# Kernel tuning notes

Hardware: AMD Instinct MI355X
Metric: run time of the kernel (lower is better)

Reference implementation:

```python
import jax, jax.numpy as jnp
import numpy as np

VOCAB = 50257
HIDDEN = 4096
DH = 512
NUM_LAYERS = 2
NUM_DRAFT = 4


def setup_inputs() -> dict:
    key = jax.random.key(0)
    ks = jax.random.split(key, 16)
    B = 64
    s_ip = 1.0 / np.sqrt(HIDDEN)
    s_h = 1.0 / np.sqrt(DH)
    inp = {
        "hidden_state": jax.random.normal(ks[0], (B, HIDDEN), dtype=jnp.float32),
        "target_ids": jax.random.randint(ks[1], (B, NUM_DRAFT), 0, VOCAB),
        "ip_w": jax.random.normal(ks[2], (DH, HIDDEN), dtype=jnp.float32) * s_ip,
        "ip_b": jnp.zeros((DH,), dtype=jnp.float32),
        "w_ih0": jax.random.normal(ks[3], (3 * DH, DH), dtype=jnp.float32) * s_h,
        "w_hh0": jax.random.normal(ks[4], (3 * DH, DH), dtype=jnp.float32) * s_h,
        "b_ih0": jax.random.normal(ks[5], (3 * DH,), dtype=jnp.float32) * s_h,
        "b_hh0": jax.random.normal(ks[6], (3 * DH,), dtype=jnp.float32) * s_h,
        "w_ih1": jax.random.normal(ks[7], (3 * DH, DH), dtype=jnp.float32) * s_h,
        "w_hh1": jax.random.normal(ks[8], (3 * DH, DH), dtype=jnp.float32) * s_h,
        "b_ih1": jax.random.normal(ks[9], (3 * DH,), dtype=jnp.float32) * s_h,
        "b_hh1": jax.random.normal(ks[10], (3 * DH,), dtype=jnp.float32) * s_h,
        "embed": jax.random.normal(ks[11], (VOCAB, DH), dtype=jnp.float32),
        "out_w": jax.random.normal(ks[12], (VOCAB, DH), dtype=jnp.float32) * s_h,
    }
    return inp


def _gru_cell(x, h, w_ih, w_hh, b_ih, b_hh):
    # PyTorch GRU cell, gate order (r, z, n)
    gi = x @ w_ih.T + b_ih
    gh = h @ w_hh.T + b_hh
    ir, iz, inn = jnp.split(gi, 3, axis=-1)
    hr, hz, hn = jnp.split(gh, 3, axis=-1)
    r = jax.nn.sigmoid(ir + hr)
    z = jax.nn.sigmoid(iz + hz)
    n = jnp.tanh(inn + r * hn)
    return (1.0 - z) * n + z * h


def reference(hidden_state, target_ids, ip_w, ip_b, w_ih0, w_hh0, b_ih0, b_hh0,
              w_ih1, w_hh1, b_ih1, b_hh1, embed, out_w):
    B = hidden_state.shape[0]
    h0 = hidden_state @ ip_w.T + ip_b           # [B, DH]
    h = [h0, h0]                                # replicated over num_layers
    x = jnp.zeros((B, DH), dtype=hidden_state.dtype)
    logits_list = []
    for step in range(NUM_DRAFT):
        h1 = _gru_cell(x, h[0], w_ih0, w_hh0, b_ih0, b_hh0)
        h2 = _gru_cell(h1, h[1], w_ih1, w_hh1, b_ih1, b_hh1)
        h = [h1, h2]
        logits = h2 @ out_w.T                   # [B, VOCAB]
        logits_list.append(logits)
        x = embed[target_ids[:, step]]          # teacher-forced next input
    return jnp.stack(logits_list, axis=1)       # [B, NUM_DRAFT, VOCAB]
```

## Files before the change

### kernel.cpp

```cpp
#include <hip/hip_runtime.h>
#include <hip/hip_bf16.h>

#define B64   64
#define DH    512
#define HID   4096
#define VOC   50257
#define NSTEP 4
#define HSZ   (B64*DH)
#define NL0   64
#define NL1   64

typedef __attribute__((ext_vector_type(8)))  short bf16x8;
typedef __attribute__((ext_vector_type(4)))  float f32x4;
typedef __attribute__((ext_vector_type(16))) float f32x16;
typedef __hip_bfloat16 bf16;

__device__ __forceinline__ bf16x8 ldg8(const bf16* p) {
    return *reinterpret_cast<const bf16x8*>(p);
}
__device__ __forceinline__ short f2bf(float x) {
    bf16 h = __float2bfloat16(x);
    return *reinterpret_cast<short*>(&h);
}
__device__ __forceinline__ bf16x8 cvt8(const float* p) {
    f32x4 a = *reinterpret_cast<const f32x4*>(p);
    f32x4 b = *reinterpret_cast<const f32x4*>(p + 4);
    bf16x8 r;
    r[0] = f2bf(a[0]); r[1] = f2bf(a[1]); r[2] = f2bf(a[2]); r[3] = f2bf(a[3]);
    r[4] = f2bf(b[0]); r[5] = f2bf(b[1]); r[6] = f2bf(b[2]); r[7] = f2bf(b[3]);
    return r;
}
__device__ __forceinline__ float sigmf(float x) { return 1.f / (1.f + __expf(-x)); }
__device__ __forceinline__ f32x4 mfma16(bf16x8 a, bf16x8 b, f32x4 c) {
    return __builtin_amdgcn_mfma_f32_16x16x32_bf16(a, b, c, 0, 0, 0);
}

__global__ __launch_bounds__(512) void k_prep(
    const float* __restrict__ hs, const float* __restrict__ ipw,
    const float* __restrict__ wi0, const float* __restrict__ wh0,
    const float* __restrict__ wi1, const float* __restrict__ wh1,
    const float* __restrict__ embed, const int* __restrict__ tids,
    bf16* __restrict__ hsb, bf16* __restrict__ ipwb,
    bf16* __restrict__ w0i, bf16* __restrict__ w0h,
    bf16* __restrict__ w1i, bf16* __restrict__ w1h,
    bf16* __restrict__ xemb)
{
    int c = blockIdx.x * 512 + threadIdx.x;
    const float* src; bf16* dst;
    if      (c < 262144) { size_t t = c;           src = ipw + t*8; dst = ipwb + t*8; }
    else if (c < 294912) { size_t t = c - 262144;  src = hs  + t*8; dst = hsb  + t*8; }
    else if (c < 393216) { size_t t = c - 294912;  src = wi0 + t*8; dst = w0i + t*8; }
    else if (c < 491520) { size_t t = c - 393216;  src = wh0 + t*8; dst = w0h + t*8; }
    else if (c < 589824) { size_t t = c - 491520;  src = wi1 + t*8; dst = w1i + t*8; }
    else if (c < 688128) { size_t t = c - 589824;  src = wh1 + t*8; dst = w1h + t*8; }
    else {
        int t = c - 688128;
        int r = t >> 6, j = t & 63;
        int s = r >> 6, b = r & 63;
        int rid = tids[b * NSTEP + s];
        src = embed + (size_t)rid * DH + j * 8;
        dst = xemb  + (size_t)r   * DH + j * 8;
    }
    *reinterpret_cast<bf16x8*>(dst) = cvt8(src);
}

__device__ __forceinline__ void barwait(int* bar, int idx, int target) {
    if (threadIdx.x == 0) {
        while (__hip_atomic_load(&bar[idx], __ATOMIC_RELAXED, __HIP_MEMORY_SCOPE_AGENT) < target)
            __builtin_amdgcn_s_sleep(1);
        (void)__hip_atomic_load(&bar[idx], __ATOMIC_ACQUIRE, __HIP_MEMORY_SCOPE_AGENT);
    }
    __syncthreads();
}
__device__ __forceinline__ void barbump(int* bar, int idx) {
    __syncthreads();
    if (threadIdx.x == 0)
        __hip_atomic_fetch_add(&bar[idx], 1, __ATOMIC_RELEASE, __HIP_MEMORY_SCOPE_AGENT);
}

__global__ __launch_bounds__(512) void k_rec(
    const bf16* __restrict__ hsb, const bf16* __restrict__ ipwb, const float* __restrict__ ipb,
    const bf16* __restrict__ w0i, const bf16* __restrict__ w0h,
    const float* __restrict__ bi0, const float* __restrict__ bh0,
    const bf16* __restrict__ w1i, const bf16* __restrict__ w1h,
    const float* __restrict__ bi1, const float* __restrict__ bh1,
    const bf16* __restrict__ xemb,
    bf16* __restrict__ h0b3, bf16* __restrict__ h1b, bf16* __restrict__ hbig,
    int* __restrict__ bar)
{
    __shared__ __align__(16) char smem[131072];
    int tid = threadIdx.x, w = tid >> 6, lane = tid & 63;
    int lr = lane & 15, q = lane >> 4;
    int bid = blockIdx.x;
    bool isL0 = bid < NL0;
    int sub = isL0 ? bid : bid - NL0;
    int dt = sub >> 1, mh = sub & 1;
    int d0 = dt * 16, M0 = mh * 32;
    int mt = w >> 2, kc = w & 3;
    int m0 = M0 + mt * 16, ml = mt * 16;
    int d = d0 + lr;
    int row = m0 + q * 4 + kc;

    if (isL0) {
        float bR0 = bi0[d] + bh0[d], bZ0 = bi0[DH+d] + bh0[DH+d];
        float biN0 = bi0[2*DH+d],    bhN0 = bh0[2*DH+d];
        float* sG = (float*)(smem + 81920);
        f32x4 zero4 = {0.f,0.f,0.f,0.f};
        float h0st;

        {
            const bf16* arow = hsb  + (size_t)(m0 + lr) * HID + kc * 1024 + q * 8;
            const bf16* brow = ipwb + (size_t)(d0 + lr) * HID + kc * 1024 + q * 8;
            f32x4 acc = zero4;
#pragma unroll 8
            for (int k0 = 0; k0 < 1024; k0 += 32)
                acc = mfma16(ldg8(arow + k0), ldg8(brow + k0), acc);
#pragma unroll
            for (int r = 0; r < 4; ++r) sG[(w*4 + r)*64 + lane] = acc[r];
            __syncthreads();
            float S = 0.f;
#pragma unroll
            for (int j = 0; j < 4; ++j) S += sG[((mt*4 + j)*4 + kc)*64 + lane];
            float v = S + ipb[d];
            h0st = v;
            bf16 vb = __float2bfloat16(v);
            h0b3[row * DH + d] = vb;
            h1b[row * DH + d] = vb;
            __syncthreads();
        }

#pragma unroll
        for (int i = 0; i < 6; ++i) {
            int c = tid + 512*i;
            int g = c >> 10, r = (c >> 6) & 15, kg = c & 63;
            const bf16* src = w0h + ((size_t)(g*DH + d0 + r))*DH + kg*8;
            int dst = g*16384 + r*1024 + ((kg*16) ^ ((r & 7) << 4));
            *reinterpret_cast<bf16x8*>(smem + dst) = ldg8(src);
        }

        float giR[NSTEP] = {0,0,0,0}, giZ[NSTEP] = {0,0,0,0}, giN[NSTEP] = {0,0,0,0};
#pragma unroll
        for (int s = 1; s < NSTEP; ++s) {
            const bf16* xr = xemb + (size_t)((s-1)*B64 + m0 + lr)*DH + kc*128 + q*8;
#pragma unroll
            for (int g = 0; g < 3; ++g) {
                const bf16* wr = w0i + (size_t)(g*DH + d0 + lr)*DH + kc*128 + q*8;
                f32x4 a = zero4;
#pragma unroll
                for (int kt = 0; kt < 4; ++kt)
                    a = mfma16(ldg8(xr + kt*32), ldg8(wr + kt*32), a);
#pragma unroll
                for (int r = 0; r < 4; ++r) sG[((g*8 + w)*4 + r)*64 + lane] = a[r];
            }
            __syncthreads();
            float sR = 0, sZ = 0, sN = 0;
#pragma unroll
            for (int j = 0; j < 4; ++j) {
                sR += sG[((0*8 + mt*4 + j)*4 + kc)*64 + lane];
                sZ += sG[((1*8 + mt*4 + j)*4 + kc)*64 + lane];
                sN += sG[((2*8 + mt*4 + j)*4 + kc)*64 + lane];
            }
            giR[s] = sR; giZ[s] = sZ; giN[s] = sN;
            __syncthreads();
        }
        barbump(bar, 0);

        for (int s = 0; s < NSTEP; ++s) {
            barwait(bar, s == 0 ? 0 : s, NL0);
            if (s == 3) barwait(bar, 8 + 0, NL1);
            const bf16* hsrc = h0b3 + (size_t)(s % 3) * HSZ;
#pragma unroll
            for (int i = 0; i < 4; ++i) {
                int c = tid + 512*i;
                int rr = c >> 6, kg = c & 63;
                int dst = 49152 + rr*1024 + ((kg*16) ^ ((rr & 7) << 4));
                *reinterpret_cast<bf16x8*>(smem + dst) =
                    ldg8(hsrc + (size_t)(M0 + rr)*DH + kg*8);
            }
            __syncthreads();
            bf16x8 af[4];
            int arow = ml + lr;
#pragma unroll
            for (int kt = 0; kt < 4; ++kt) {
                int ke = (kc*128 + kt*32 + q*8) * 2;
                af[kt] = *reinterpret_cast<const bf16x8*>(
                    smem + 49152 + arow*1024 + (ke ^ ((arow & 7) << 4)));
            }
            f32x4 ag[3];
#pragma unroll
            for (int g = 0; g < 3; ++g) {
                f32x4 a = zero4;
#pragma unroll
                for (int kt = 0; kt < 4; ++kt) {
                    int ke = (kc*128 + kt*32 + q*8) * 2;
                    bf16x8 b = *reinterpret_cast<const bf16x8*>(
                        smem + g*16384 + lr*1024 + (ke ^ ((lr & 7) << 4)));
                    a = mfma16(af[kt], b, a);
                }
                ag[g] = a;
            }
#pragma unroll
            for (int g = 0; g < 3; ++g)
#pragma unroll
                for (int r = 0; r < 4; ++r)
                    sG[((g*8 + w)*4 + r)*64 + lane] = ag[g][r];
            __syncthreads();
            float G0 = 0, G1 = 0, GN = 0;
#pragma unroll
            for (int j = 0; j < 4; ++j) {
                G0 += sG[((0*8 + mt*4 + j)*4 + kc)*64 + lane];
                G1 += sG[((1*8 + mt*4 + j)*4 + kc)*64 + lane];
                GN += sG[((2*8 + mt*4 + j)*4 + kc)*64 + lane];
            }
            float rg = sigmf(G0 + giR[s] + bR0);
            float zg = sigmf(G1 + giZ[s] + bZ0);
            float ng = tanhf(giN[s] + biN0 + rg * (GN + bhN0));
            h0st = (1.f - zg) * ng + zg * h0st;
            h0b3[(size_t)((s + 1) % 3) * HSZ + row * DH + d] = __float2bfloat16(h0st);
            barbump(bar, 1 + s);
        }
    } else {
        float bR1 = bi1[d] + bh1[d], bZ1 = bi1[DH+d] + bh1[DH+d];
        float biN1 = bi1[2*DH+d],    bhN1 = bh1[2*DH+d];
        float* sG = (float*)(smem + 98304);
        f32x4 zero4 = {0.f,0.f,0.f,0.f};

#pragma unroll
        for (int i = 0; i < 12; ++i) {
            int c = tid + 512*i;
            int mi = c / 3072, rem = c % 3072;
            int g = rem >> 10, r = (rem >> 6) & 15, kg = rem & 63;
            const bf16* base = mi ? w1i : w1h;
            const bf16* src = base + ((size_t)(g*DH + d0 + r))*DH + kg*8;
            int dst = mi*49152 + g*16384 + r*1024 + ((kg*16) ^ ((r & 7) << 4));
            *reinterpret_cast<bf16x8*>(smem + dst) = ldg8(src);
        }
        barwait(bar, 0, NL0);
        float h1st = __bfloat162float(h1b[row * DH + d]);

        int c1 = 0;
        for (int s = 0; s < NSTEP; ++s) {
            barwait(bar, 1 + s, NL0);
            if (s > 0) barwait(bar, 8 + s - 1, NL1);
            const bf16* h0r = h0b3 + (size_t)((s + 1) % 3) * HSZ
                              + (size_t)(m0 + lr)*DH + kc*128 + q*8;
            bf16x8 a0[4];
#pragma unroll
            for (int kt = 0; kt < 4; ++kt) a0[kt] = ldg8(h0r + kt*32);
            const bf16* h1src = h1b + (size_t)c1 * HSZ;
#pragma unroll
            for (int i = 0; i < 4; ++i) {
                int c = tid + 512*i;
                int rr = c >> 6, kg = c & 63;
                int dst = 98304 + rr*1024 + ((kg*16) ^ ((rr & 7) << 4));
                *reinterpret_cast<bf16x8*>(smem + dst) =
                    ldg8(h1src + (size_t)(M0 + rr)*DH + kg*8);
            }
            __syncthreads();
            bf16x8 a1[4];
            int arow = ml + lr;
#pragma unroll
            for (int kt = 0; kt < 4; ++kt) {
                int ke = (kc*128 + kt*32 + q*8) * 2;
                a1[kt] = *reinterpret_cast<const bf16x8*>(
                    smem + 98304 + arow*1024 + (ke ^ ((arow & 7) << 4)));
            }
            f32x4 comb0 = zero4, comb1 = zero4, hN = zero4, iN = zero4;
#pragma unroll
            for (int g = 0; g < 3; ++g) {
                f32x4 aH = zero4, aI = zero4;
#pragma unroll
                for (int kt = 0; kt < 4; ++kt) {
                    int ke = (kc*128 + kt*32 + q*8) * 2;
                    bf16x8 bH = *reinterpret_cast<const bf16x8*>(
                        smem + g*16384 + lr*1024 + (ke ^ ((lr & 7) << 4)));
                    bf16x8 bI = *reinterpret_cast<const bf16x8*>(
                        smem + 49152 + g*16384 + lr*1024 + (ke ^ ((lr & 7) << 4)));
                    aH = mfma16(a1[kt], bH, aH);
                    aI = mfma16(a0[kt], bI, aI);
                }
                if (g == 0) { comb0 = aH; comb0[0] += aI[0]; comb0[1] += aI[1]; comb0[2] += aI[2]; comb0[3] += aI[3]; }
                else if (g == 1) { comb1 = aH; comb1[0] += aI[0]; comb1[1] += aI[1]; comb1[2] += aI[2]; comb1[3] += aI[3]; }
                else { hN = aH; iN = aI; }
            }
            __syncthreads();
#pragma unroll
            for (int r = 0; r < 4; ++r) {
                sG[((0*8 + w)*4 + r)*64 + lane] = comb0[r];
                sG[((1*8 + w)*4 + r)*64 + lane] = comb1[r];
                sG[((2*8 + w)*4 + r)*64 + lane] = hN[r];
                sG[((3*8 + w)*4 + r)*64 + lane] = iN[r];
            }
            __syncthreads();
            float GR = 0, GZ = 0, GhN = 0, GiN = 0;
#pragma unroll
            for (int j = 0; j < 4; ++j) {
                GR  += sG[((0*8 + mt*4 + j)*4 + kc)*64 + lane];
                GZ  += sG[((1*8 + mt*4 + j)*4 + kc)*64 + lane];
                GhN += sG[((2*8 + mt*4 + j)*4 + kc)*64 + lane];
                GiN += sG[((3*8 + mt*4 + j)*4 + kc)*64 + lane];
            }
            float rg = sigmf(GR + bR1);
            float zg = sigmf(GZ + bZ1);
            float ng = tanhf(GiN + biN1 + rg * (GhN + bhN1));
            h1st = (1.f - zg) * ng + zg * h1st;
            bf16 hvb = __float2bfloat16(h1st);
            h1b[(size_t)(c1 ^ 1) * HSZ + row * DH + d] = hvb;
            hbig[(size_t)(row * NSTEP + s) * DH + d] = hvb;
            c1 ^= 1;
            barbump(bar, 8 + s);
        }
    }
}

__global__ __launch_bounds__(256) void k_logits(
    const bf16* __restrict__ hbig, const float* __restrict__ outw, float* __restrict__ out)
{
    __shared__ __align__(16) bf16 sA[256 * 64];
    int t = threadIdx.x, w = t >> 6, lane = t & 63;
    int l32 = lane & 31, e = lane >> 5;
    int mh = w >> 1;
    int n = blockIdx.x * 64 + (w & 1) * 32 + l32;
    int nr = n < VOC ? n : VOC - 1;
    const float* brow = outw + (size_t)nr * DH;

    f32x16 acc[4];
#pragma unroll
    for (int i = 0; i < 4; ++i)
#pragma unroll
        for (int j = 0; j < 16; ++j) acc[i][j] = 0.f;

    for (int k0 = 0; k0 < DH; k0 += 64) {
#pragma unroll
        for (int i = 0; i < 8; ++i) {
            int c = i * 256 + t;
            int m = c >> 3, j = c & 7;
            *reinterpret_cast<bf16x8*>(&sA[m * 64 + ((j ^ (m & 7)) << 3)]) =
                ldg8(hbig + (size_t)m * DH + k0 + j * 8);
        }
        __syncthreads();
#pragma unroll
        for (int kk = 0; kk < 64; kk += 16) {
            bf16x8 bfrag = cvt8(brow + k0 + kk + e * 8);
            int g = (kk >> 3) + e;
#pragma unroll
            for (int mt2 = 0; mt2 < 4; ++mt2) {
                int r = (mh * 4 + mt2) * 32 + l32;
                bf16x8 afrag = *reinterpret_cast<const bf16x8*>(
                    &sA[r * 64 + ((g ^ (r & 7)) << 3)]);
                acc[mt2] = __builtin_amdgcn_mfma_f32_32x32x16_bf16(afrag, bfrag, acc[mt2], 0, 0, 0);
            }
        }
        __syncthreads();
    }
    if (n < VOC) {
#pragma unroll
        for (int mt2 = 0; mt2 < 4; ++mt2)
#pragma unroll
            for (int reg = 0; reg < 16; ++reg) {
                int m = (mh * 4 + mt2) * 32 + (reg & 3) + 8 * (reg >> 2) + 4 * e;
                out[(size_t)m * VOC + n] = acc[mt2][reg];
            }
    }
}

extern "C" void kernel_launch(void* const* d_in, const int* in_sizes, int n_in,
                              void* d_out, int out_size, void* d_ws, size_t ws_size,
                              hipStream_t stream) {
    const float* hs   = (const float*)d_in[0];
    const int*   tids = (const int*)d_in[1];
    const float* ipw  = (const float*)d_in[2];
    const float* ipb  = (const float*)d_in[3];
    const float* wih0 = (const float*)d_in[4];
    const float* whh0 = (const float*)d_in[5];
    const float* bih0 = (const float*)d_in[6];
    const float* bhh0 = (const float*)d_in[7];
    const float* wih1 = (const float*)d_in[8];
    const float* whh1 = (const float*)d_in[9];
    const float* bih1 = (const float*)d_in[10];
    const float* bhh1 = (const float*)d_in[11];
    const float* embed = (const float*)d_in[12];
    const float* outw  = (const float*)d_in[13];
    float* out = (float*)d_out;

    char* ws = (char*)d_ws;
    int*  bar  = (int*) (ws + 0);
    bf16* hsb  = (bf16*)(ws + 1024);
    bf16* ipwb = (bf16*)(ws + 525312);
    bf16* w0i  = (bf16*)(ws + 4719616);
    bf16* w0h  = (bf16*)(ws + 6292480);
    bf16* w1i  = (bf16*)(ws + 7865344);
    bf16* w1h  = (bf16*)(ws + 9438208);
    bf16* xemb = (bf16*)(ws + 11011072);
    bf16* h0b3 = (bf16*)(ws + 11207680);
    bf16* h1b  = (bf16*)(ws + 11404288);
    bf16* hbig = (bf16*)(ws + 11535360);

    hipMemsetAsync(bar, 0, 256, stream);

    k_prep<<<1368, 512, 0, stream>>>(hs, ipw, wih0, whh0, wih1, whh1, embed, tids,
                                     hsb, ipwb, w0i, w0h, w1i, w1h, xemb);

    k_rec<<<NL0 + NL1, 512, 0, stream>>>(hsb, ipwb, ipb,
                                         w0i, w0h, bih0, bhh0,
                                         w1i, w1h, bih1, bhh1,
                                         xemb, h0b3, h1b, hbig, bar);

    k_logits<<<(VOC + 63) / 64, 256, 0, stream>>>(hbig, outw, out);
}
```

Before: 355.7 us.

## Restructure logits GEMM: stage out_w in double-buffered LDS, read activations from global

The logits kernel now stages the fp32 out_w tile, converted to bf16, into a double-buffered swizzled LDS buffer, and prefetches the next K-slice while the current one runs MFMA. The small hbig activation matrix is read straight from global memory (L2) into registers instead of LDS. Blocks grow to 512 threads with 8 waves, each holding 2 accumulator tiles instead of 4. The aim is to coalesce the large out_w stream, overlap its load with compute, and raise occupancy. In exchange, every wave makes repeated global reads of hbig.

```diff
diff --git a/kernel.cpp b/kernel.cpp
--- a/kernel.cpp
+++ b/kernel.cpp
@@ -30,9 +30,18 @@
     r[4] = f2bf(b[0]); r[5] = f2bf(b[1]); r[6] = f2bf(b[2]); r[7] = f2bf(b[3]);
     return r;
 }
+__device__ __forceinline__ bf16x8 cvt8r(f32x4 a, f32x4 b) {
+    bf16x8 r;
+    r[0] = f2bf(a[0]); r[1] = f2bf(a[1]); r[2] = f2bf(a[2]); r[3] = f2bf(a[3]);
+    r[4] = f2bf(b[0]); r[5] = f2bf(b[1]); r[6] = f2bf(b[2]); r[7] = f2bf(b[3]);
+    return r;
+}
 __device__ __forceinline__ float sigmf(float x) { return 1.f / (1.f + __expf(-x)); }
 __device__ __forceinline__ f32x4 mfma16(bf16x8 a, bf16x8 b, f32x4 c) {
     return __builtin_amdgcn_mfma_f32_16x16x32_bf16(a, b, c, 0, 0, 0);
+}
+__device__ __forceinline__ f32x16 mfma32(bf16x8 a, bf16x8 b, f32x16 c) {
+    return __builtin_amdgcn_mfma_f32_32x32x16_bf16(a, b, c, 0, 0, 0);
 }
 
 __global__ __launch_bounds__(512) void k_prep(
@@ -313,53 +322,71 @@
     }
 }
 
-__global__ __launch_bounds__(256) void k_logits(
+__global__ __launch_bounds__(512, 4) void k_logits(
     const bf16* __restrict__ hbig, const float* __restrict__ outw, float* __restrict__ out)
 {
-    __shared__ __align__(16) bf16 sA[256 * 64];
+    __shared__ __align__(16) char sB[2][8192];
     int t = threadIdx.x, w = t >> 6, lane = t & 63;
     int l32 = lane & 31, e = lane >> 5;
-    int mh = w >> 1;
-    int n = blockIdx.x * 64 + (w & 1) * 32 + l32;
-    int nr = n < VOC ? n : VOC - 1;
-    const float* brow = outw + (size_t)nr * DH;
-
-    f32x16 acc[4];
-#pragma unroll
-    for (int i = 0; i < 4; ++i)
+    int ng = w & 1, mq = w >> 1;
+    int n0 = blockIdx.x * 64;
+    int n = n0 + ng * 32 + l32;
+
+    int srow = t >> 3, skg = t & 7;
+    int srow_c = n0 + srow; if (srow_c > VOC - 1) srow_c = VOC - 1;
+    const float* gsrc = outw + (size_t)srow_c * DH + skg * 8;
+    int soff = skg * 1024 + ((srow ^ skg) << 4);
+
+    f32x16 acc[2];
+#pragma unroll
+    for (int i = 0; i < 2; ++i)
 #pragma unroll
         for (int j = 0; j < 16; ++j) acc[i][j] = 0.f;
 
+    {
+        f32x4 ga = *reinterpret_cast<const f32x4*>(gsrc);
+        f32x4 gb = *reinterpret_cast<const f32x4*>(gsrc + 4);
+        *reinterpret_cast<bf16x8*>(&sB[0][soff]) = cvt8r(ga, gb);
+    }
+    __syncthreads();
+
+    int cur = 0;
+    const bf16* arowbase = hbig + (size_t)(mq * 64 + l32) * DH + e * 8;
     for (int k0 = 0; k0 < DH; k0 += 64) {
-#pragma unroll
-        for (int i = 0; i < 8; ++i) {
-            int c = i * 256 + t;
-            int m = c >> 3, j = c & 7;
-            *reinterpret_cast<bf16x8*>(&sA[m * 64 + ((j ^ (m & 7)) << 3)]) =
-                ldg8(hbig + (size_t)m * DH + k0 + j * 8);
-        }
-        __syncthreads();
-#pragma unroll
-        for (int kk = 0; kk < 64; kk += 16) {
-            bf16x8 bfrag = cvt8(brow + k0 + kk + e * 8);
-            int g = (kk >> 3) + e;
-#pragma unroll
-            for (int mt2 = 0; mt2 < 4; ++mt2) {
-                int r = (mh * 4 + mt2) * 32 + l32;
-                bf16x8 afrag = *reinterpret_cast<const bf16x8*>(
-                    &sA[r * 64 + ((g ^ (r & 7)) << 3)]);
-                acc[mt2] = __builtin_amdgcn_mfma_f32_32x32x16_bf16(afrag, bfrag, acc[mt2], 0, 0, 0);
-            }
-        }
-        __syncthreads();
+        bool more = (k0 + 64 < DH);
+        f32x4 ga, gb;
+        if (more) {
+            ga = *reinterpret_cast<const f32x4*>(gsrc + k0 + 64);
+            gb = *reinterpret_cast<const f32x4*>(gsrc + k0 + 64 + 4);
+        }
+        bf16x8 areg[2][4];
+#pragma unroll
+        for (int mt = 0; mt < 2; ++mt)
+#pragma unroll
+            for (int kk = 0; kk < 4; ++kk)
+                areg[mt][kk] = ldg8(arowbase + (size_t)mt * 32 * DH + k0 + kk * 16);
+#pragma unroll
+        for (int kk = 0; kk < 4; ++kk) {
+            int kg = kk * 2 + e;
+            int rr = ng * 32 + l32;
+            bf16x8 bfrag = *reinterpret_cast<const bf16x8*>(
+                &sB[cur][kg * 1024 + ((rr ^ kg) << 4)]);
+            acc[0] = mfma32(areg[0][kk], bfrag, acc[0]);
+            acc[1] = mfma32(areg[1][kk], bfrag, acc[1]);
+        }
+        if (more) {
+            *reinterpret_cast<bf16x8*>(&sB[cur ^ 1][soff]) = cvt8r(ga, gb);
+            __syncthreads();
+            cur ^= 1;
+        }
     }
     if (n < VOC) {
 #pragma unroll
-        for (int mt2 = 0; mt2 < 4; ++mt2)
+        for (int mt = 0; mt < 2; ++mt)
 #pragma unroll
             for (int reg = 0; reg < 16; ++reg) {
-                int m = (mh * 4 + mt2) * 32 + (reg & 3) + 8 * (reg >> 2) + 4 * e;
-                out[(size_t)m * VOC + n] = acc[mt2][reg];
+                int m = mq * 64 + mt * 32 + (reg & 3) + 8 * (reg >> 2) + 4 * e;
+                out[(size_t)m * VOC + n] = acc[mt][reg];
             }
     }
 }
@@ -406,5 +433,5 @@
                                          w1i, w1h, bih1, bhh1,
                                          xemb, h0b3, h1b, hbig, bar);
 
-    k_logits<<<(VOC + 63) / 64, 256, 0, stream>>>(hbig, outw, out);
-}
+    k_logits<<<(VOC + 63) / 64, 512, 0, stream>>>(hbig, outw, out);
+}
```

Result: slower. 376.4 us (+5.8%).

## Convert out_w to bf16 on idle CUs during recurrence, feed logits bf16

Applied to the files above, without the earlier changes.

Adds 128 extra blocks to the recurrent kernel that convert the fp32 output projection weight to bf16 in workspace while the 128 GRU blocks run their sequential steps. The logits kernel then reads bf16 weights directly, halving its weight traffic and dropping per-fragment conversion, and preloads four B fragments per k-chunk. It depends on the workspace being large enough and falls back to the fp32 path otherwise. Risk: the converter blocks compete for bandwidth with the latency-bound recurrence and could delay the spin-barrier GRU blocks if they are not all co-resident.

```diff
diff --git a/kernel.cpp b/kernel.cpp
--- a/kernel.cpp
+++ b/kernel.cpp
@@ -9,6 +9,7 @@
 #define HSZ   (B64*DH)
 #define NL0   64
 #define NL1   64
+#define NCV   128
 
 typedef __attribute__((ext_vector_type(8)))  short bf16x8;
 typedef __attribute__((ext_vector_type(4)))  float f32x4;
@@ -33,6 +34,9 @@
 __device__ __forceinline__ float sigmf(float x) { return 1.f / (1.f + __expf(-x)); }
 __device__ __forceinline__ f32x4 mfma16(bf16x8 a, bf16x8 b, f32x4 c) {
     return __builtin_amdgcn_mfma_f32_16x16x32_bf16(a, b, c, 0, 0, 0);
+}
+__device__ __forceinline__ f32x16 mfma32(bf16x8 a, bf16x8 b, f32x16 c) {
+    return __builtin_amdgcn_mfma_f32_32x32x16_bf16(a, b, c, 0, 0, 0);
 }
 
 __global__ __launch_bounds__(512) void k_prep(
@@ -86,12 +90,22 @@
     const float* __restrict__ bi1, const float* __restrict__ bh1,
     const bf16* __restrict__ xemb,
     bf16* __restrict__ h0b3, bf16* __restrict__ h1b, bf16* __restrict__ hbig,
-    int* __restrict__ bar)
+    int* __restrict__ bar,
+    const float* __restrict__ outw_f, bf16* __restrict__ outwb)
 {
     __shared__ __align__(16) char smem[131072];
     int tid = threadIdx.x, w = tid >> 6, lane = tid & 63;
+    int bid = blockIdx.x;
+
+    if (bid >= NL0 + NL1) {
+        const size_t total = (size_t)VOC * DH / 8;
+        size_t i = (size_t)(bid - NL0 - NL1) * 512 + tid;
+        for (; i < total; i += (size_t)NCV * 512)
+            *reinterpret_cast<bf16x8*>(outwb + i * 8) = cvt8(outw_f + i * 8);
+        return;
+    }
+
     int lr = lane & 15, q = lane >> 4;
-    int bid = blockIdx.x;
     bool isL0 = bid < NL0;
     int sub = isL0 ? bid : bid - NL0;
     int dt = sub >> 1, mh = sub & 1;
@@ -313,7 +327,61 @@
     }
 }
 
-__global__ __launch_bounds__(256) void k_logits(
+__global__ __launch_bounds__(256) void k_logits_b(
+    const bf16* __restrict__ hbig, const bf16* __restrict__ outwb, float* __restrict__ out)
+{
+    __shared__ __align__(16) bf16 sA[256 * 64];
+    int t = threadIdx.x, w = t >> 6, lane = t & 63;
+    int l32 = lane & 31, e = lane >> 5;
+    int mh = w >> 1;
+    int n = blockIdx.x * 64 + (w & 1) * 32 + l32;
+    int nr = n < VOC ? n : VOC - 1;
+    const bf16* brow = outwb + (size_t)nr * DH;
+
+    f32x16 acc[4];
+#pragma unroll
+    for (int i = 0; i < 4; ++i)
+#pragma unroll
+        for (int j = 0; j < 16; ++j) acc[i][j] = 0.f;
+
+    for (int k0 = 0; k0 < DH; k0 += 64) {
+#pragma unroll
+        for (int i = 0; i < 8; ++i) {
+            int c = i * 256 + t;
+            int m = c >> 3, j = c & 7;
+            *reinterpret_cast<bf16x8*>(&sA[m * 64 + ((j ^ (m & 7)) << 3)]) =
+                ldg8(hbig + (size_t)m * DH + k0 + j * 8);
+        }
+        __syncthreads();
+        bf16x8 bfv[4];
+#pragma unroll
+        for (int i = 0; i < 4; ++i)
+            bfv[i] = ldg8(brow + k0 + i * 16 + e * 8);
+#pragma unroll
+        for (int i = 0; i < 4; ++i) {
+            int g = i * 2 + e;
+#pragma unroll
+            for (int mt2 = 0; mt2 < 4; ++mt2) {
+                int r = (mh * 4 + mt2) * 32 + l32;
+                bf16x8 afrag = *reinterpret_cast<const bf16x8*>(
+                    &sA[r * 64 + ((g ^ (r & 7)) << 3)]);
+                acc[mt2] = mfma32(afrag, bfv[i], acc[mt2]);
+            }
+        }
+        __syncthreads();
+    }
+    if (n < VOC) {
+#pragma unroll
+        for (int mt2 = 0; mt2 < 4; ++mt2)
+#pragma unroll
+            for (int reg = 0; reg < 16; ++reg) {
+                int m = (mh * 4 + mt2) * 32 + (reg & 3) + 8 * (reg >> 2) + 4 * e;
+                out[(size_t)m * VOC + n] = acc[mt2][reg];
+            }
+    }
+}
+
+__global__ __launch_bounds__(256) void k_logits_f(
     const bf16* __restrict__ hbig, const float* __restrict__ outw, float* __restrict__ out)
 {
     __shared__ __align__(16) bf16 sA[256 * 64];
@@ -348,7 +416,7 @@
                 int r = (mh * 4 + mt2) * 32 + l32;
                 bf16x8 afrag = *reinterpret_cast<const bf16x8*>(
                     &sA[r * 64 + ((g ^ (r & 7)) << 3)]);
-                acc[mt2] = __builtin_amdgcn_mfma_f32_32x32x16_bf16(afrag, bfrag, acc[mt2], 0, 0, 0);
+                acc[mt2] = mfma32(afrag, bfrag, acc[mt2]);
             }
         }
         __syncthreads();
@@ -395,16 +463,24 @@
     bf16* h0b3 = (bf16*)(ws + 11207680);
     bf16* h1b  = (bf16*)(ws + 11404288);
     bf16* hbig = (bf16*)(ws + 11535360);
+    bf16* outwb = (bf16*)(ws + 11798528);
+    size_t need = 11798528 + (size_t)VOC * DH * 2;
+    bool bf16B = (ws_size >= need);
 
     hipMemsetAsync(bar, 0, 256, stream);
 
     k_prep<<<1368, 512, 0, stream>>>(hs, ipw, wih0, whh0, wih1, whh1, embed, tids,
                                      hsb, ipwb, w0i, w0h, w1i, w1h, xemb);
 
-    k_rec<<<NL0 + NL1, 512, 0, stream>>>(hsb, ipwb, ipb,
-                                         w0i, w0h, bih0, bhh0,
-                                         w1i, w1h, bih1, bhh1,
-                                         xemb, h0b3, h1b, hbig, bar);
-
-    k_logits<<<(VOC + 63) / 64, 256, 0, stream>>>(hbig, outw, out);
-}
+    int grid_rec = bf16B ? (NL0 + NL1 + NCV) : (NL0 + NL1);
+    k_rec<<<grid_rec, 512, 0, stream>>>(hsb, ipwb, ipb,
+                                        w0i, w0h, bih0, bhh0,
+                                        w1i, w1h, bih1, bhh1,
+                                        xemb, h0b3, h1b, hbig, bar,
+                                        outw, outwb);
+
+    if (bf16B)
+        k_logits_b<<<(VOC + 63) / 64, 256, 0, stream>>>(hbig, outwb, out);
+    else
+        k_logits_f<<<(VOC + 63) / 64, 256, 0, stream>>>(hbig, outw, out);
+}
```

Result: faster. 333.1 us (-6.4%).
